# Kernel optimization log

Measured on AMD Instinct MI355X. Metric: run time of the kernel, lower is better.

Reference implementation:

```python
import jax, jax.numpy as jnp
import numpy as np

MIN_NORM = 1e-5
C = 1.0
CLIP_R = 1.0

@jax.custom_vjp
def riemannian_grad_fix(x):
    # identity fwd; bwd rescales grad by the inverse conformal metric (hyptorch RiemannianGradient)
    return x

def _rgf_fwd(x):
    return x, x

def _rgf_bwd(x, g):
    scale = (1.0 - C * jnp.sum(x * x, axis=-1, keepdims=True)) ** 2 / 4.0
    return (g * scale,)

riemannian_grad_fix.defvjp(_rgf_fwd, _rgf_bwd)

def expmap0(u, c):
    sqrt_c = jnp.sqrt(c)
    u_norm = jnp.maximum(jnp.linalg.norm(u, axis=-1, keepdims=True), MIN_NORM)
    return jnp.tanh(sqrt_c * u_norm) * u / (sqrt_c * u_norm)

def project(x, c):
    norm = jnp.maximum(jnp.linalg.norm(x, axis=-1, keepdims=True), MIN_NORM)
    maxnorm = (1.0 - 1e-3) / jnp.sqrt(c)
    return jnp.where(norm > maxnorm, x / norm * maxnorm, x)

def to_poincare(x, c):
    # clip_r=1 clipping, then expmap0 + project; riemannian grad fix is identity in fwd
    x_norm = jnp.linalg.norm(x, axis=-1, keepdims=True) + 1e-5
    fac = jnp.minimum(jnp.ones_like(x_norm), CLIP_R / x_norm)
    x = x * fac
    return riemannian_grad_fix(project(expmap0(x, c), c))

def hyperbolic_softmax(X, A, P, c):
    # X: (B, d) points on the ball; A, P: (n, d)
    sqrt_c = jnp.sqrt(c)
    p2 = jnp.sum(P * P, axis=1)                       # (n,)
    a_norm = jnp.linalg.norm(A, axis=1)               # (n,)
    lam = 2.0 / (1.0 - c * p2)                        # (n,)
    k = lam * a_norm / sqrt_c                         # (n,)
    # batched mobius addition (-P) (+) X  -> (n, B, d)
    xy = jnp.einsum('nd,bd->nb', -P, X)               # (n, B)
    y2 = jnp.sum(X * X, axis=1)[None, :]              # (1, B)
    x2 = p2[:, None]                                  # (n, 1)
    num_coef = 1.0 + 2.0 * c * xy + c * y2            # (n, B)
    mob = num_coef[..., None] * (-P)[:, None, :] + (1.0 - c * x2)[..., None] * X[None, :, :]
    denom = 1.0 + 2.0 * c * xy + (c ** 2) * x2 * y2   # (n, B)
    mob = mob / (denom[..., None] + 1e-5)
    num = 2.0 * sqrt_c * jnp.einsum('nbd,nd->nb', mob, A)
    den = a_norm[:, None] * (1.0 - c * jnp.sum(mob * mob, axis=2))
    logit = k[:, None] * jnp.arcsinh(num / den)       # (n, B)
    return logit.T                                    # (B, n)

def setup_inputs() -> dict:
    key = jax.random.key(0)
    k1, k2, k3 = jax.random.split(key, 3)
    B, N, D = 2048, 512, 256
    x = jax.random.normal(k1, (B, D), dtype=jnp.float32)
    a_vals = jax.random.normal(k2, (N, D), dtype=jnp.float32) * 0.05
    p_vals = jax.random.normal(k3, (N, D), dtype=jnp.float32) * 0.05
    return {"x": x, "a_vals": a_vals, "p_vals": p_vals}

def reference(x, a_vals, p_vals):
    c = jnp.asarray(C, dtype=x.dtype)
    xb = to_poincare(x, c)
    p_poincare = expmap0(p_vals, c)                                   # (n, d)
    conformal = 1.0 - c * jnp.sum(p_poincare ** 2, axis=1, keepdims=True)  # (n, 1)
    a_poincare = a_vals * conformal                                   # (n, d)
    return hyperbolic_softmax(xb, a_poincare, p_poincare, c)          # (B, n)
```

## Files before the change

### kernel.cpp

```cpp
#include <hip/hip_runtime.h>
#include <math.h>

#define BB 2048
#define NN 512
#define DD 256

typedef __attribute__((ext_vector_type(8))) _Float16 f16x8;
typedef __attribute__((ext_vector_type(4))) float f32x4;

#define MFMA_F16 __builtin_amdgcn_mfma_f32_16x16x32_f16

__device__ __forceinline__ ushort f2h(float f) {
    union { _Float16 h; ushort u; } c; c.h = (_Float16)f; return c.u;
}
__device__ __forceinline__ uint2 pack4h(f32x4 v, float s) {
    uint2 r;
    r.x = (unsigned)f2h(v.x * s) | ((unsigned)f2h(v.y * s) << 16);
    r.y = (unsigned)f2h(v.z * s) | ((unsigned)f2h(v.w * s) << 16);
    return r;
}
__device__ __forceinline__ float fast_asinh(float z) {
    float az = fabsf(z);
    float r = __logf(az + sqrtf(fmaf(az, az, 1.0f)));
    return copysignf(r, z);
}

__global__ __launch_bounds__(256) void hmlr_transform(
    const float* __restrict__ x, const float* __restrict__ a_vals,
    const float* __restrict__ p_vals,
    ushort* __restrict__ Xf, ushort* __restrict__ Pf, ushort* __restrict__ Af,
    float* __restrict__ y2, float* __restrict__ p2s, float* __restrict__ pas,
    float* __restrict__ ans, float* __restrict__ ks)
{
    const int lane = threadIdx.x & 63;
    const int wid  = blockIdx.x * 4 + (threadIdx.x >> 6);
    const int e0   = lane * 4;

    if (wid < BB) {
        const int r = wid;
        f32x4 v = *(const f32x4*)&x[(size_t)r * DD + e0];
        float ss = v.x * v.x + v.y * v.y + v.z * v.z + v.w * v.w;
        #pragma unroll
        for (int m = 32; m; m >>= 1) ss += __shfl_xor(ss, m, 64);
        float norm0 = sqrtf(ss);
        float fac = fminf(1.0f, 1.0f / (norm0 + 1e-5f));
        float u = fmaxf(norm0 * fac, 1e-5f);
        float th = tanhf(u);
        float en = fmaxf(th, 1e-5f);
        float wgt = (en > 0.999f) ? (0.999f / en) : 1.0f;
        float s = fac * (th / u) * wgt;
        if (lane == 0) { float fn = th * wgt; y2[r] = fn * fn; }
        int es = e0 ^ ((r & 7) << 3);
        *(uint2*)&Xf[(size_t)r * DD + es] = pack4h(v, s);
    } else {
        const int n = wid - BB;
        f32x4 pv = *(const f32x4*)&p_vals[(size_t)n * DD + e0];
        f32x4 av = *(const f32x4*)&a_vals[(size_t)n * DD + e0];
        float sp = pv.x * pv.x + pv.y * pv.y + pv.z * pv.z + pv.w * pv.w;
        float sa = av.x * av.x + av.y * av.y + av.z * av.z + av.w * av.w;
        float sx = pv.x * av.x + pv.y * av.y + pv.z * av.z + pv.w * av.w;
        #pragma unroll
        for (int m = 32; m; m >>= 1) {
            sp += __shfl_xor(sp, m, 64);
            sa += __shfl_xor(sa, m, 64);
            sx += __shfl_xor(sx, m, 64);
        }
        float u = fmaxf(sqrtf(sp), 1e-5f);
        float th = tanhf(u);
        float spp = th / u;
        float p2 = th * th;
        float conf = 1.0f - p2;
        if (lane == 0) {
            p2s[n] = p2;
            pas[n] = spp * conf * sx;
            float an = sqrtf(sa) * conf;
            ans[n] = an;
            ks[n] = (2.0f / conf) * an;
        }
        int es = e0 ^ ((n & 7) << 3);
        *(uint2*)&Pf[(size_t)n * DD + es] = pack4h(pv, spp);
        *(uint2*)&Af[(size_t)n * DD + es] = pack4h(av, conf);
    }
}

__global__ __launch_bounds__(512) void hmlr_gemm(
    const ushort* __restrict__ Xf, const ushort* __restrict__ Pf,
    const ushort* __restrict__ Af,
    const float* __restrict__ y2, const float* __restrict__ p2s,
    const float* __restrict__ pas, const float* __restrict__ ans,
    const float* __restrict__ ks, float* __restrict__ out)
{
    extern __shared__ ushort T[];

    const int t    = threadIdx.x;
    const int lane = t & 63;
    const int w    = t >> 6;
    const int bid  = blockIdx.x;
    const int xcd  = bid & 7;
    const int j    = bid >> 3;
    const int b0   = (xcd * 4 + (j >> 3)) * 64;
    const int n0   = (j & 7) * 64;
    const int wr   = w >> 2;
    const int wc   = w & 3;

    const ushort* bases[3] = {Xf, Pf, Af};

    f32x4 axy0 = {0.f,0.f,0.f,0.f}, axy1 = {0.f,0.f,0.f,0.f};
    f32x4 axa0 = {0.f,0.f,0.f,0.f}, axa1 = {0.f,0.f,0.f,0.f};

    auto stage = [&](int buf, int s) {
        #pragma unroll
        for (int i = 0; i < 3; ++i) {
            int g = w * 3 + i;
            int mat = g >> 3;
            int sub = g & 7;
            int grow = (mat == 0 ? b0 : n0) + sub * 8 + (lane >> 3);
            const ushort* src = bases[mat] + (size_t)grow * DD + s * 64 + (lane & 7) * 8;
            const ushort* dst = T + (((buf * 3 + mat) * 64 + sub * 8) * 64);
            __builtin_amdgcn_global_load_lds(
                (const __attribute__((address_space(1))) unsigned int*)(const void*)src,
                (__attribute__((address_space(3))) unsigned int*)(void*)dst,
                16, 0, 0);
        }
    };

    const int ram = wr * 32 + (lane & 15);
    const int rbn = wc * 16 + (lane & 15);
    const int gb  = (lane >> 4) << 4;

    stage(0, 0);

    const int n = n0 + rbn;
    float p2 = p2s[n], pa = pas[n], an = ans[n], kk = ks[n];
    float yv[8];
    #pragma unroll
    for (int m = 0; m < 2; ++m)
        #pragma unroll
        for (int rg = 0; rg < 4; ++rg)
            yv[m * 4 + rg] = y2[b0 + wr * 32 + m * 16 + (lane >> 4) * 4 + rg];
    asm volatile("" :: "v"(p2), "v"(pa), "v"(an), "v"(kk));
    #pragma unroll
    for (int i = 0; i < 8; ++i) asm volatile("" :: "v"(yv[i]));

    for (int s = 0; s < 4; ++s) {
        __syncthreads();
        if (s < 3) stage((s + 1) & 1, s + 1);
        const int bf = s & 1;
        #pragma unroll
        for (int ksl = 0; ksl < 2; ++ksl) {
            const int kb = ksl * 64 + gb;
            const ushort* base = T + (bf * 3 * 64 * 64);
            const char* x0 = (const char*)(base + (0 * 64 + ram) * 64);
            const int sa0 = kb ^ ((ram & 7) << 4);
            const int sb0 = kb ^ ((rbn & 7) << 4);
            const int sa1 = kb ^ (((ram + 16) & 7) << 4);
            f16x8 xf0 = *(const f16x8*)(x0 + sa0);
            f16x8 xf1 = *(const f16x8*)(x0 + 16 * 128 + sa1);
            f16x8 pf  = *(const f16x8*)((const char*)(base + (1 * 64 + rbn) * 64) + sb0);
            f16x8 af  = *(const f16x8*)((const char*)(base + (2 * 64 + rbn) * 64) + sb0);
            axy0 = MFMA_F16(xf0, pf, axy0, 0, 0, 0);
            axy1 = MFMA_F16(xf1, pf, axy1, 0, 0, 0);
            axa0 = MFMA_F16(xf0, af, axa0, 0, 0, 0);
            axa1 = MFMA_F16(xf1, af, axa1, 0, 0, 0);
        }
    }

    #pragma unroll
    for (int m = 0; m < 2; ++m) {
        f32x4 acc_xy = m ? axy1 : axy0;
        f32x4 acc_xa = m ? axa1 : axa0;
        #pragma unroll
        for (int rg = 0; rg < 4; ++rg) {
            int b = b0 + wr * 32 + m * 16 + (lane >> 4) * 4 + rg;
            float yy  = yv[m * 4 + rg];
            float xy  = -acc_xy[rg];
            float xa  =  acc_xa[rg];
            float dnm = 1.f + 2.f * xy + p2 * yy + 1e-5f;
            float alpha = (1.f + 2.f * xy + yy) / dnm;
            float beta  = (1.f - p2) / dnm;
            float num  = 2.f * (beta * xa - alpha * pa);
            float mob2 = alpha * alpha * p2 + beta * beta * yy
                       + 2.f * alpha * beta * xy;
            float den  = an * (1.f - mob2);
            out[(size_t)b * NN + n] = kk * fast_asinh(num / den);
        }
    }
}

extern "C" void kernel_launch(void* const* d_in, const int* in_sizes, int n_in,
                              void* d_out, int out_size, void* d_ws, size_t ws_size,
                              hipStream_t stream) {
    const float* x      = (const float*)d_in[0];
    const float* a_vals = (const float*)d_in[1];
    const float* p_vals = (const float*)d_in[2];
    float* out = (float*)d_out;

    ushort* Xf = (ushort*)d_ws;
    ushort* Pf = Xf + (size_t)BB * DD;
    ushort* Af = Pf + (size_t)NN * DD;
    float*  y2  = (float*)(Af + (size_t)NN * DD);
    float*  p2s = y2 + BB;
    float*  pas = p2s + NN;
    float*  ans = pas + NN;
    float*  ks  = ans + NN;

    (void)hipFuncSetAttribute(reinterpret_cast<const void*>(hmlr_gemm),
                              hipFuncAttributeMaxDynamicSharedMemorySize, 49152);

    hipLaunchKernelGGL(hmlr_transform, dim3((BB + NN) / 4), dim3(256), 0, stream,
                       x, a_vals, p_vals, Xf, Pf, Af, y2, p2s, pas, ans, ks);
    hipLaunchKernelGGL(hmlr_gemm, dim3(256), dim3(512), 49152, stream,
                       Xf, Pf, Af, y2, p2s, pas, ans, ks, out);
}
```

Baseline: 16.57 us.

## Load full K extent into LDS at once, removing double-buffered pipeline

The GEMM kernel now issues all twelve global-to-LDS loads per wave up front, covering the whole 256-wide K dimension of the X, P and A tiles, then waits on one barrier and runs eight unrolled MFMA steps. This replaces the four-stage double-buffered loop, which paid a barrier per stage and exposed load latency in small chunks. LDS use per block doubles to 96 KB. With one block per CU this should not cost occupancy, but the MFMA work can no longer overlap the tail of the loads.

```diff
diff --git a/kernel.cpp b/kernel.cpp
--- a/kernel.cpp
+++ b/kernel.cpp
@@ -105,30 +105,23 @@
 
     const ushort* bases[3] = {Xf, Pf, Af};
 
-    f32x4 axy0 = {0.f,0.f,0.f,0.f}, axy1 = {0.f,0.f,0.f,0.f};
-    f32x4 axa0 = {0.f,0.f,0.f,0.f}, axa1 = {0.f,0.f,0.f,0.f};
-
-    auto stage = [&](int buf, int s) {
-        #pragma unroll
-        for (int i = 0; i < 3; ++i) {
-            int g = w * 3 + i;
-            int mat = g >> 3;
-            int sub = g & 7;
-            int grow = (mat == 0 ? b0 : n0) + sub * 8 + (lane >> 3);
-            const ushort* src = bases[mat] + (size_t)grow * DD + s * 64 + (lane & 7) * 8;
-            const ushort* dst = T + (((buf * 3 + mat) * 64 + sub * 8) * 64);
-            __builtin_amdgcn_global_load_lds(
-                (const __attribute__((address_space(1))) unsigned int*)(const void*)src,
-                (__attribute__((address_space(3))) unsigned int*)(void*)dst,
-                16, 0, 0);
-        }
-    };
+    #pragma unroll
+    for (int i = 0; i < 12; ++i) {
+        int g = w * 12 + i;
+        int mat = g >> 5;
+        int c = g & 31;
+        int grow = (mat == 0 ? b0 : n0) + c * 2 + (lane >> 5);
+        const ushort* src = bases[mat] + (size_t)grow * DD + (lane & 31) * 8;
+        const ushort* dst = T + ((mat * 64 + c * 2) * 256);
+        __builtin_amdgcn_global_load_lds(
+            (const __attribute__((address_space(1))) unsigned int*)(const void*)src,
+            (__attribute__((address_space(3))) unsigned int*)(void*)dst,
+            16, 0, 0);
+    }
 
     const int ram = wr * 32 + (lane & 15);
     const int rbn = wc * 16 + (lane & 15);
-    const int gb  = (lane >> 4) << 4;
-
-    stage(0, 0);
+    const int ge  = (lane >> 4) * 8;
 
     const int n = n0 + rbn;
     float p2 = p2s[n], pa = pas[n], an = ans[n], kk = ks[n];
@@ -142,27 +135,30 @@
     #pragma unroll
     for (int i = 0; i < 8; ++i) asm volatile("" :: "v"(yv[i]));
 
-    for (int s = 0; s < 4; ++s) {
-        __syncthreads();
-        if (s < 3) stage((s + 1) & 1, s + 1);
-        const int bf = s & 1;
-        #pragma unroll
-        for (int ksl = 0; ksl < 2; ++ksl) {
-            const int kb = ksl * 64 + gb;
-            const ushort* base = T + (bf * 3 * 64 * 64);
-            const char* x0 = (const char*)(base + (0 * 64 + ram) * 64);
-            const int sa0 = kb ^ ((ram & 7) << 4);
-            const int sb0 = kb ^ ((rbn & 7) << 4);
-            const int sa1 = kb ^ (((ram + 16) & 7) << 4);
-            f16x8 xf0 = *(const f16x8*)(x0 + sa0);
-            f16x8 xf1 = *(const f16x8*)(x0 + 16 * 128 + sa1);
-            f16x8 pf  = *(const f16x8*)((const char*)(base + (1 * 64 + rbn) * 64) + sb0);
-            f16x8 af  = *(const f16x8*)((const char*)(base + (2 * 64 + rbn) * 64) + sb0);
-            axy0 = MFMA_F16(xf0, pf, axy0, 0, 0, 0);
-            axy1 = MFMA_F16(xf1, pf, axy1, 0, 0, 0);
-            axa0 = MFMA_F16(xf0, af, axa0, 0, 0, 0);
-            axa1 = MFMA_F16(xf1, af, axa1, 0, 0, 0);
-        }
+    __syncthreads();
+
+    f32x4 axy0 = {0.f,0.f,0.f,0.f}, axy1 = {0.f,0.f,0.f,0.f};
+    f32x4 axa0 = {0.f,0.f,0.f,0.f}, axa1 = {0.f,0.f,0.f,0.f};
+    const int swzA = (ram & 7) << 3;
+    const int swzB = (rbn & 7) << 3;
+    const ushort* x0r = T + (size_t)ram * 256;
+    const ushort* x1r = T + (size_t)(ram + 16) * 256;
+    const ushort* pr  = T + (size_t)(64 + rbn) * 256;
+    const ushort* ar  = T + (size_t)(128 + rbn) * 256;
+
+    #pragma unroll
+    for (int q = 0; q < 8; ++q) {
+        int f = q * 32 + ge;
+        int pA = f ^ swzA;
+        int pB = f ^ swzB;
+        f16x8 xf0 = *(const f16x8*)(x0r + pA);
+        f16x8 xf1 = *(const f16x8*)(x1r + pA);
+        f16x8 pf  = *(const f16x8*)(pr + pB);
+        f16x8 af  = *(const f16x8*)(ar + pB);
+        axy0 = MFMA_F16(xf0, pf, axy0, 0, 0, 0);
+        axy1 = MFMA_F16(xf1, pf, axy1, 0, 0, 0);
+        axa0 = MFMA_F16(xf0, af, axa0, 0, 0, 0);
+        axa1 = MFMA_F16(xf1, af, axa1, 0, 0, 0);
     }
 
     #pragma unroll
@@ -205,10 +201,10 @@
     float*  ks  = ans + NN;
 
     (void)hipFuncSetAttribute(reinterpret_cast<const void*>(hmlr_gemm),
-                              hipFuncAttributeMaxDynamicSharedMemorySize, 49152);
+                              hipFuncAttributeMaxDynamicSharedMemorySize, 98304);
 
     hipLaunchKernelGGL(hmlr_transform, dim3((BB + NN) / 4), dim3(256), 0, stream,
                        x, a_vals, p_vals, Xf, Pf, Af, y2, p2s, pas, ans, ks);
-    hipLaunchKernelGGL(hmlr_gemm, dim3(256), dim3(512), 49152, stream,
+    hipLaunchKernelGGL(hmlr_gemm, dim3(256), dim3(512), 98304, stream,
                        Xf, Pf, Af, y2, p2s, pas, ans, ks, out);
 }
```

Measured after the change: 16.39 us, median of 2. No clear change (-1.1%).
